# Optimization experiments

Measured on AMD Instinct MI355X. Metric: run time of the kernel, lower is better.

The kernel has to match this reference:

```python
import jax, jax.numpy as jnp
import numpy as np
import math

B, H, S, D = 4, 16, 2048, 128

def setup_inputs() -> dict:
    key = jax.random.key(0)
    kq, kk, kv = jax.random.split(key, 3)
    Q = jax.random.normal(kq, (B, H, S, D), dtype=jnp.float32)
    K = jax.random.normal(kk, (B, H, S, D), dtype=jnp.float32)
    V = jax.random.normal(kv, (B, H, S, D), dtype=jnp.float32)
    return {"Q": Q, "K": K, "V": V}

def reference(Q, K, V):
    # scores: [B, H, S, S]
    scale = 1.0 / math.sqrt(Q.shape[-1])
    scores = jnp.einsum('bhqd,bhkd->bhqk', Q, K) * scale
    attn = jax.nn.softmax(scores, axis=-1)
    return jnp.einsum('bhqk,bhkd->bhqd', attn, V)
```

## Files before the change

kernel.cpp:

```cpp
#include <hip/hip_runtime.h>
#include <stdint.h>

#define BATCH 4
#define HEADS 16
#define SEQ 2048
#define DIM 128

constexpr int QBLK  = 256;
constexpr int KVB   = 64;
constexpr int NKT   = SEQ / KVB;
constexpr int TILEB = KVB * DIM * 2;
constexpr int NBH   = BATCH * HEADS;

constexpr int K0 = 0;
constexpr int K1 = 16384;
constexpr int K2 = 32768;
constexpr int V0 = 49152;
constexpr int V1 = 65536;
constexpr int V2 = 81920;

typedef __bf16 bf16x8 __attribute__((ext_vector_type(8)));
typedef float  f32x4  __attribute__((ext_vector_type(4)));
typedef float  f32x16 __attribute__((ext_vector_type(16)));
typedef unsigned int uint32;

typedef const __attribute__((address_space(1))) void* gas_t;
typedef __attribute__((address_space(3))) void* las_t;

__device__ __forceinline__ uint32 packbf2(float a, float b) {
  union { __bf16 h[2]; uint32 u; } c;
  c.h[0] = (__bf16)a; c.h[1] = (__bf16)b;
  return c.u;
}

__global__ __launch_bounds__(256)
void prepass(const float* __restrict__ Kg, const float* __restrict__ Vg,
             char* __restrict__ Kws, char* __restrict__ Vws)
{
  __shared__ __bf16 sVt[DIM * 72];
  const int tile = blockIdx.x;
  const int tid  = threadIdx.x;
  const float* Ksrc = Kg + (size_t)tile * KVB * DIM;
  const float* Vsrc = Vg + (size_t)tile * KVB * DIM;
  char* kdst = Kws + (size_t)tile * TILEB;
  char* vdst = Vws + (size_t)tile * TILEB;

#pragma unroll
  for (int c = 0; c < 4; ++c) {
    const int flat8 = (c * 256 + tid) * 8;
    const int kv = flat8 >> 7, d0 = flat8 & 127;
    union { float4 f; float a[4]; } x0, x1;
    x0.f = *(const float4*)(Ksrc + flat8);
    x1.f = *(const float4*)(Ksrc + flat8 + 4);
    bf16x8 kx;
#pragma unroll
    for (int j = 0; j < 4; ++j) { kx[j] = (__bf16)x0.a[j]; kx[4 + j] = (__bf16)x1.a[j]; }
    *(bf16x8*)(kdst + kv * 256 + ((2 * d0) ^ ((kv & 15) << 4))) = kx;

    union { float4 f; float a[4]; } v0, v1;
    v0.f = *(const float4*)(Vsrc + flat8);
    v1.f = *(const float4*)(Vsrc + flat8 + 4);
#pragma unroll
    for (int j = 0; j < 8; ++j) {
      const int d = d0 + j;
      const float vv = (j < 4) ? v0.a[j] : v1.a[j - 4];
      sVt[d * 72 + (kv ^ (((d >> 3) & 7) << 3))] = (__bf16)vv;
    }
  }
  __syncthreads();
#pragma unroll
  for (int c = 0; c < 4; ++c) {
    const int flat8 = (c * 256 + tid) * 8;
    const int d = flat8 >> 6, kv0 = flat8 & 63;
    bf16x8 row = *(const bf16x8*)(&sVt[d * 72 + (kv0 ^ (((d >> 3) & 7) << 3))]);
    *(bf16x8*)(vdst + (d & 63) * 256 +
               ((((d >> 6) << 7) | (2 * kv0)) ^ (((d & 63) & 15) << 4))) = row;
  }
}


#define QK_HALF(KOFF)                                                            \
  {                                                                              \
    s = (f32x16)0.0f;                                                            \
    __builtin_amdgcn_s_setprio(1);                                               \
    _Pragma("unroll")                                                            \
    for (int k = 0; k < 8; ++k) {                                                \
      bf16x8 kf = *(const bf16x8*)(smem + (KOFF) + akv[k]);                      \
      s = __builtin_amdgcn_mfma_f32_32x32x16_bf16(kf, qf[k], s, 0, 0, 0);        \
    }                                                                            \
    __builtin_amdgcn_s_setprio(0);                                               \
  }

#define PV_BODY(VOFF)                                                            \
  {                                                                              \
    __builtin_amdgcn_s_setprio(1);                                               \
    _Pragma("unroll")                                                            \
    for (int td = 0; td < 4; ++td) {                                             \
      _Pragma("unroll")                                                          \
      for (int k = 0; k < 4; ++k) {                                              \
        const int ab = (td >> 1) ? (akv[k] ^ 128) : akv[k];                      \
        bf16x8 vf = *(const bf16x8*)(smem + (VOFF) + ab + (td & 1) * 8192);      \
        oacc[td] = __builtin_amdgcn_mfma_f32_32x32x16_bf16(vf, pb[k], oacc[td], 0, 0, 0); \
      }                                                                          \
    }                                                                            \
    __builtin_amdgcn_s_setprio(0);                                               \
  }

#define EXP_HALF(PB0)                                                            \
  {                                                                              \
    uint32 pk[8];                                                                \
    float rs = 0.f;                                                              \
    _Pragma("unroll")                                                            \
    for (int i = 0; i < 8; ++i) {                                                \
      float a0 = __builtin_amdgcn_exp2f(s[2*i]);                                 \
      float a1 = __builtin_amdgcn_exp2f(s[2*i+1]);                               \
      rs += a0 + a1;                                                             \
      pk[i] = packbf2(a0, a1);                                                   \
    }                                                                            \
    lrp += rs;                                                                   \
    _Pragma("unroll")                                                            \
    for (int h = 0; h < 2; ++h) {                                                \
      auto r0 = __builtin_amdgcn_permlane32_swap((int)pk[h*4+0], (int)pk[h*4+2], false, false); \
      auto r1 = __builtin_amdgcn_permlane32_swap((int)pk[h*4+1], (int)pk[h*4+3], false, false); \
      union { uint32 u[4]; bf16x8 v; } w;                                        \
      w.u[0] = (uint32)r0[0]; w.u[1] = (uint32)r1[0];                            \
      w.u[2] = (uint32)r0[1]; w.u[3] = (uint32)r1[1];                            \
      pb[(PB0) + h] = w.v;                                                       \
    }                                                                            \
  }

#define STAGE_K(DST, kt)                                                         \
  do {                                                                           \
    const char* p_ = Kt + (size_t)(kt) * TILEB;                                  \
    _Pragma("unroll")                                                            \
    for (int c_ = 0; c_ < 2; ++c_) {                                             \
      const int od_ = c_ * 8192 + wid * 1024;                                    \
      __builtin_amdgcn_global_load_lds((gas_t)(p_ + od_ + lane * 16),            \
                                       (las_t)(smem + (DST) + od_), 16, 0, 0);   \
    }                                                                            \
  } while (0)

#define STAGE_V(DST, kt)                                                         \
  do {                                                                           \
    const char* p_ = Vt + (size_t)(kt) * TILEB;                                  \
    _Pragma("unroll")                                                            \
    for (int c_ = 0; c_ < 2; ++c_) {                                             \
      const int od_ = c_ * 8192 + wid * 1024;                                    \
      __builtin_amdgcn_global_load_lds((gas_t)(p_ + od_ + lane * 16),            \
                                       (las_t)(smem + (DST) + od_), 16, 0, 0);   \
    }                                                                            \
  } while (0)

#define CBAR(VMN)                                                                \
  asm volatile("s_waitcnt vmcnt(" #VMN ")" ::: "memory");                        \
  __builtin_amdgcn_s_barrier();                                                  \
  __builtin_amdgcn_sched_barrier(0);

#define PHASE(T, KR, VR, KW, VW, DOK, DOV, VMN)                                  \
  {                                                                              \
    if (DOK) STAGE_K(KW, (T) + 2);                                               \
    if (DOV) STAGE_V(VW, (T) + 1);                                               \
    QK_HALF(KR)                                                                  \
    PV_BODY(VR)                                                                  \
    EXP_HALF(0)                                                                  \
    QK_HALF((KR) + 8192)                                                         \
    EXP_HALF(2)                                                                  \
    CBAR(VMN)                                                                    \
  }

__global__ __launch_bounds__(512, 2)
void attn_fwd(const float* __restrict__ Qg, float* __restrict__ Og,
              const char* __restrict__ Kws, const char* __restrict__ Vws)
{
  __shared__ __align__(16) char smem[98304];

  const int tid  = threadIdx.x;
  const int lane = tid & 63;
  const int wid  = tid >> 6;
  const int l    = lane & 31;
  const int hi   = lane >> 5;

  const int bid = blockIdx.x;
  const int swz = ((bid & 7) << 6) + (bid >> 3);
  const int bh  = swz >> 3;
  const int qb  = swz & 7;

  const float* Qb = Qg + (size_t)bh * SEQ * DIM;
  float*       Ob = Og + (size_t)bh * SEQ * DIM;
  const char*  Kt = Kws + (size_t)bh * NKT * TILEB;
  const char*  Vt = Vws + (size_t)bh * NKT * TILEB;

  const int q0 = qb * QBLK + wid * 32;

  int akv[8];
#pragma unroll
  for (int k = 0; k < 8; ++k)
    akv[k] = l * 256 + ((k * 32 + hi * 16) ^ ((l & 15) << 4));

  const float qscale = 0.08838834764831845f * 1.4426950408889634f;
  bf16x8 qf[8];
  {
    const float* qrow = Qb + (size_t)(q0 + l) * DIM;
#pragma unroll
    for (int k = 0; k < 8; ++k) {
      const int d0 = k * 16 + hi * 8;
      union { float4 f; float a[4]; } x0, x1;
      x0.f = *(const float4*)(qrow + d0);
      x1.f = *(const float4*)(qrow + d0 + 4);
      bf16x8 f;
#pragma unroll
      for (int j = 0; j < 4; ++j) {
        f[j]     = (__bf16)(x0.a[j] * qscale);
        f[4 + j] = (__bf16)(x1.a[j] * qscale);
      }
      qf[k] = f;
    }
  }

  float lrp = 0.f;
  f32x16 s;
  bf16x8 pb[4];
  f32x16 oacc[4];
#pragma unroll
  for (int t = 0; t < 4; ++t) oacc[t] = (f32x16)0.0f;

  STAGE_K(K0, 0);
  STAGE_K(K1, 1);
  STAGE_V(V0, 0);
  CBAR(4)

  {
    STAGE_K(K2, 2);
    STAGE_V(V1, 1);
    QK_HALF(K0)
    EXP_HALF(0)
    QK_HALF(K0 + 8192)
    EXP_HALF(2)
    CBAR(4)
  }

#pragma unroll 1
  for (int b = 1; b <= 25; b += 3) {
    PHASE(b + 0, K1, V0, K0, V2, 1, 1, 4)
    PHASE(b + 1, K2, V1, K1, V0, 1, 1, 4)
    PHASE(b + 2, K0, V2, K2, V1, 1, 1, 4)
  }
  PHASE(28, K1, V0, K0, V2, 1, 1, 4)
  PHASE(29, K2, V1, K1, V0, 1, 1, 4)
  PHASE(30, K0, V2, K0, V1, 0, 1, 2)
  PHASE(31, K1, V0, K0, V0, 0, 0, 0)
  PV_BODY(V1);

  const float lrow = lrp + __shfl_xor(lrp, 32, 64);
  const float inv = 1.0f / lrow;
  float* sO = (float*)smem;
#pragma unroll
  for (int pass = 0; pass < 2; ++pass) {
    if (pass) __syncthreads();
#pragma unroll
    for (int td2 = 0; td2 < 2; ++td2) {
      const int td = pass * 2 + td2;
#pragma unroll
      for (int rq = 0; rq < 4; ++rq) {
        const int dp = td2 * 32 + rq * 8 + hi * 4;
        f32x4 o;
        o[0] = oacc[td][rq * 4 + 0] * inv;
        o[1] = oacc[td][rq * 4 + 1] * inv;
        o[2] = oacc[td][rq * 4 + 2] * inv;
        o[3] = oacc[td][rq * 4 + 3] * inv;
        *(f32x4*)(&sO[(wid * 32 + l) * 64 + (dp ^ ((l & 15) << 2))]) = o;
      }
    }
    __syncthreads();
#pragma unroll
    for (int c = 0; c < 8; ++c) {
      const int flat4 = (c * 512 + tid) * 4;
      const int q = flat4 >> 6, dp0 = flat4 & 63;
      f32x4 o = *(const f32x4*)(&sO[q * 64 + (dp0 ^ ((q & 15) << 2))]);
      *(f32x4*)(Ob + (size_t)(qb * QBLK + q) * DIM + pass * 64 + dp0) = o;
    }
  }
}

extern "C" void kernel_launch(void* const* d_in, const int* in_sizes, int n_in,
                              void* d_out, int out_size, void* d_ws, size_t ws_size,
                              hipStream_t stream) {
  const float* Q = (const float*)d_in[0];
  const float* K = (const float*)d_in[1];
  const float* V = (const float*)d_in[2];
  float* O = (float*)d_out;
  char* Kws = (char*)d_ws;
  char* Vws = Kws + (size_t)NBH * NKT * TILEB;
  prepass<<<NBH * NKT, 256, 0, stream>>>(K, V, Kws, Vws);
  attn_fwd<<<NBH * 8, 512, 0, stream>>>(Q, O, Kws, Vws);
}
```

Measured before the change: 188.5 us.

## Give each wave two 32-row query tiles and halve the block size

Each wave now handles 64 query rows as two 32-row sub-tiles that share every K and V fragment loaded from LDS. This halves LDS reads per MFMA, and the block shrinks to 4 waves (256 threads) covering the same 256-row query block. Staging loops and wait counts are adjusted for the smaller thread count. The doubled accumulators and score registers raise register pressure, and launch bounds drop to 1 block of 256 threads, which may cut occupancy and latency hiding.

```diff
diff --git a/kernel.cpp b/kernel.cpp
--- a/kernel.cpp
+++ b/kernel.cpp
@@ -79,45 +79,47 @@
 }
 
 
-#define QK_HALF(KOFF)                                                            \
+#define QK_HALF2(KOFF)                                                           \
   {                                                                              \
-    s = (f32x16)0.0f;                                                            \
+    sA = (f32x16)0.0f; sB = (f32x16)0.0f;                                        \
     __builtin_amdgcn_s_setprio(1);                                               \
     _Pragma("unroll")                                                            \
     for (int k = 0; k < 8; ++k) {                                                \
       bf16x8 kf = *(const bf16x8*)(smem + (KOFF) + akv[k]);                      \
-      s = __builtin_amdgcn_mfma_f32_32x32x16_bf16(kf, qf[k], s, 0, 0, 0);        \
+      sA = __builtin_amdgcn_mfma_f32_32x32x16_bf16(kf, qfA[k], sA, 0, 0, 0);     \
+      sB = __builtin_amdgcn_mfma_f32_32x32x16_bf16(kf, qfB[k], sB, 0, 0, 0);     \
     }                                                                            \
     __builtin_amdgcn_s_setprio(0);                                               \
   }
 
-#define PV_BODY(VOFF)                                                            \
+#define PV_BODY2(VOFF)                                                           \
   {                                                                              \
     __builtin_amdgcn_s_setprio(1);                                               \
     _Pragma("unroll")                                                            \
-    for (int td = 0; td < 4; ++td) {                                             \
+    for (int k = 0; k < 4; ++k) {                                                \
       _Pragma("unroll")                                                          \
-      for (int k = 0; k < 4; ++k) {                                              \
+      for (int td = 0; td < 4; ++td) {                                           \
         const int ab = (td >> 1) ? (akv[k] ^ 128) : akv[k];                      \
         bf16x8 vf = *(const bf16x8*)(smem + (VOFF) + ab + (td & 1) * 8192);      \
-        oacc[td] = __builtin_amdgcn_mfma_f32_32x32x16_bf16(vf, pb[k], oacc[td], 0, 0, 0); \
+        oaccA[td] = __builtin_amdgcn_mfma_f32_32x32x16_bf16(vf, pbA[k], oaccA[td], 0, 0, 0); \
+        oaccB[td] = __builtin_amdgcn_mfma_f32_32x32x16_bf16(vf, pbB[k], oaccB[td], 0, 0, 0); \
       }                                                                          \
     }                                                                            \
     __builtin_amdgcn_s_setprio(0);                                               \
   }
 
-#define EXP_HALF(PB0)                                                            \
+#define EXP_ONE(S, PB, PB0, LRP)                                                 \
   {                                                                              \
     uint32 pk[8];                                                                \
     float rs = 0.f;                                                              \
     _Pragma("unroll")                                                            \
     for (int i = 0; i < 8; ++i) {                                                \
-      float a0 = __builtin_amdgcn_exp2f(s[2*i]);                                 \
-      float a1 = __builtin_amdgcn_exp2f(s[2*i+1]);                               \
+      float a0 = __builtin_amdgcn_exp2f(S[2*i]);                                 \
+      float a1 = __builtin_amdgcn_exp2f(S[2*i+1]);                               \
       rs += a0 + a1;                                                             \
       pk[i] = packbf2(a0, a1);                                                   \
     }                                                                            \
-    lrp += rs;                                                                   \
+    LRP += rs;                                                                   \
     _Pragma("unroll")                                                            \
     for (int h = 0; h < 2; ++h) {                                                \
       auto r0 = __builtin_amdgcn_permlane32_swap((int)pk[h*4+0], (int)pk[h*4+2], false, false); \
@@ -125,7 +127,7 @@
       union { uint32 u[4]; bf16x8 v; } w;                                        \
       w.u[0] = (uint32)r0[0]; w.u[1] = (uint32)r1[0];                            \
       w.u[2] = (uint32)r0[1]; w.u[3] = (uint32)r1[1];                            \
-      pb[(PB0) + h] = w.v;                                                       \
+      PB[(PB0) + h] = w.v;                                                       \
     }                                                                            \
   }
 
@@ -133,8 +135,8 @@
   do {                                                                           \
     const char* p_ = Kt + (size_t)(kt) * TILEB;                                  \
     _Pragma("unroll")                                                            \
-    for (int c_ = 0; c_ < 2; ++c_) {                                             \
-      const int od_ = c_ * 8192 + wid * 1024;                                    \
+    for (int c_ = 0; c_ < 4; ++c_) {                                             \
+      const int od_ = c_ * 4096 + wid * 1024;                                    \
       __builtin_amdgcn_global_load_lds((gas_t)(p_ + od_ + lane * 16),            \
                                        (las_t)(smem + (DST) + od_), 16, 0, 0);   \
     }                                                                            \
@@ -144,8 +146,8 @@
   do {                                                                           \
     const char* p_ = Vt + (size_t)(kt) * TILEB;                                  \
     _Pragma("unroll")                                                            \
-    for (int c_ = 0; c_ < 2; ++c_) {                                             \
-      const int od_ = c_ * 8192 + wid * 1024;                                    \
+    for (int c_ = 0; c_ < 4; ++c_) {                                             \
+      const int od_ = c_ * 4096 + wid * 1024;                                    \
       __builtin_amdgcn_global_load_lds((gas_t)(p_ + od_ + lane * 16),            \
                                        (las_t)(smem + (DST) + od_), 16, 0, 0);   \
     }                                                                            \
@@ -160,15 +162,17 @@
   {                                                                              \
     if (DOK) STAGE_K(KW, (T) + 2);                                               \
     if (DOV) STAGE_V(VW, (T) + 1);                                               \
-    QK_HALF(KR)                                                                  \
-    PV_BODY(VR)                                                                  \
-    EXP_HALF(0)                                                                  \
-    QK_HALF((KR) + 8192)                                                         \
-    EXP_HALF(2)                                                                  \
+    QK_HALF2(KR)                                                                 \
+    PV_BODY2(VR)                                                                 \
+    EXP_ONE(sA, pbA, 0, lrpA)                                                    \
+    EXP_ONE(sB, pbB, 0, lrpB)                                                    \
+    QK_HALF2((KR) + 8192)                                                        \
+    EXP_ONE(sA, pbA, 2, lrpA)                                                    \
+    EXP_ONE(sB, pbB, 2, lrpB)                                                    \
     CBAR(VMN)                                                                    \
   }
 
-__global__ __launch_bounds__(512, 2)
+__global__ __launch_bounds__(256, 1)
 void attn_fwd(const float* __restrict__ Qg, float* __restrict__ Og,
               const char* __restrict__ Kws, const char* __restrict__ Vws)
 {
@@ -190,7 +194,7 @@
   const char*  Kt = Kws + (size_t)bh * NKT * TILEB;
   const char*  Vt = Vws + (size_t)bh * NKT * TILEB;
 
-  const int q0 = qb * QBLK + wid * 32;
+  const int q0 = qb * QBLK + wid * 64;
 
   int akv[8];
 #pragma unroll
@@ -198,61 +202,71 @@
     akv[k] = l * 256 + ((k * 32 + hi * 16) ^ ((l & 15) << 4));
 
   const float qscale = 0.08838834764831845f * 1.4426950408889634f;
-  bf16x8 qf[8];
+  bf16x8 qfA[8], qfB[8];
   {
-    const float* qrow = Qb + (size_t)(q0 + l) * DIM;
+    const float* qrowA = Qb + (size_t)(q0 + l) * DIM;
+    const float* qrowB = Qb + (size_t)(q0 + 32 + l) * DIM;
 #pragma unroll
     for (int k = 0; k < 8; ++k) {
       const int d0 = k * 16 + hi * 8;
-      union { float4 f; float a[4]; } x0, x1;
-      x0.f = *(const float4*)(qrow + d0);
-      x1.f = *(const float4*)(qrow + d0 + 4);
-      bf16x8 f;
+      union { float4 f; float a[4]; } x0, x1, y0, y1;
+      x0.f = *(const float4*)(qrowA + d0);
+      x1.f = *(const float4*)(qrowA + d0 + 4);
+      y0.f = *(const float4*)(qrowB + d0);
+      y1.f = *(const float4*)(qrowB + d0 + 4);
+      bf16x8 fa, fb;
 #pragma unroll
       for (int j = 0; j < 4; ++j) {
-        f[j]     = (__bf16)(x0.a[j] * qscale);
-        f[4 + j] = (__bf16)(x1.a[j] * qscale);
+        fa[j]     = (__bf16)(x0.a[j] * qscale);
+        fa[4 + j] = (__bf16)(x1.a[j] * qscale);
+        fb[j]     = (__bf16)(y0.a[j] * qscale);
+        fb[4 + j] = (__bf16)(y1.a[j] * qscale);
       }
-      qf[k] = f;
+      qfA[k] = fa;
+      qfB[k] = fb;
     }
   }
 
-  float lrp = 0.f;
-  f32x16 s;
-  bf16x8 pb[4];
-  f32x16 oacc[4];
-#pragma unroll
-  for (int t = 0; t < 4; ++t) oacc[t] = (f32x16)0.0f;
+  float lrpA = 0.f, lrpB = 0.f;
+  f32x16 sA, sB;
+  bf16x8 pbA[4], pbB[4];
+  f32x16 oaccA[4], oaccB[4];
+#pragma unroll
+  for (int t = 0; t < 4; ++t) { oaccA[t] = (f32x16)0.0f; oaccB[t] = (f32x16)0.0f; }
 
   STAGE_K(K0, 0);
   STAGE_K(K1, 1);
   STAGE_V(V0, 0);
-  CBAR(4)
+  CBAR(8)
 
   {
     STAGE_K(K2, 2);
     STAGE_V(V1, 1);
-    QK_HALF(K0)
-    EXP_HALF(0)
-    QK_HALF(K0 + 8192)
-    EXP_HALF(2)
-    CBAR(4)
+    QK_HALF2(K0)
+    EXP_ONE(sA, pbA, 0, lrpA)
+    EXP_ONE(sB, pbB, 0, lrpB)
+    QK_HALF2(K0 + 8192)
+    EXP_ONE(sA, pbA, 2, lrpA)
+    EXP_ONE(sB, pbB, 2, lrpB)
+    CBAR(8)
   }
 
 #pragma unroll 1
   for (int b = 1; b <= 25; b += 3) {
-    PHASE(b + 0, K1, V0, K0, V2, 1, 1, 4)
-    PHASE(b + 1, K2, V1, K1, V0, 1, 1, 4)
-    PHASE(b + 2, K0, V2, K2, V1, 1, 1, 4)
-  }
-  PHASE(28, K1, V0, K0, V2, 1, 1, 4)
-  PHASE(29, K2, V1, K1, V0, 1, 1, 4)
-  PHASE(30, K0, V2, K0, V1, 0, 1, 2)
+    PHASE(b + 0, K1, V0, K0, V2, 1, 1, 8)
+    PHASE(b + 1, K2, V1, K1, V0, 1, 1, 8)
+    PHASE(b + 2, K0, V2, K2, V1, 1, 1, 8)
+  }
+  PHASE(28, K1, V0, K0, V2, 1, 1, 8)
+  PHASE(29, K2, V1, K1, V0, 1, 1, 8)
+  PHASE(30, K0, V2, K0, V1, 0, 1, 4)
   PHASE(31, K1, V0, K0, V0, 0, 0, 0)
-  PV_BODY(V1);
-
-  const float lrow = lrp + __shfl_xor(lrp, 32, 64);
-  const float inv = 1.0f / lrow;
+  PV_BODY2(V1);
+
+  const float lrowA = lrpA + __shfl_xor(lrpA, 32, 64);
+  const float lrowB = lrpB + __shfl_xor(lrpB, 32, 64);
+  const float invA = 1.0f / lrowA;
+  const float invB = 1.0f / lrowB;
   float* sO = (float*)smem;
 #pragma unroll
   for (int pass = 0; pass < 2; ++pass) {
@@ -263,19 +277,21 @@
 #pragma unroll
       for (int rq = 0; rq < 4; ++rq) {
         const int dp = td2 * 32 + rq * 8 + hi * 4;
-        f32x4 o;
-        o[0] = oacc[td][rq * 4 + 0] * inv;
-        o[1] = oacc[td][rq * 4 + 1] * inv;
-        o[2] = oacc[td][rq * 4 + 2] * inv;
-        o[3] = oacc[td][rq * 4 + 3] * inv;
-        *(f32x4*)(&sO[(wid * 32 + l) * 64 + (dp ^ ((l & 15) << 2))]) = o;
+        f32x4 oa, ob;
+#pragma unroll
+        for (int j = 0; j < 4; ++j) {
+          oa[j] = oaccA[td][rq * 4 + j] * invA;
+          ob[j] = oaccB[td][rq * 4 + j] * invB;
+        }
+        *(f32x4*)(&sO[(wid * 64 + l) * 64 + (dp ^ ((l & 15) << 2))])      = oa;
+        *(f32x4*)(&sO[(wid * 64 + 32 + l) * 64 + (dp ^ ((l & 15) << 2))]) = ob;
       }
     }
     __syncthreads();
 #pragma unroll
-    for (int c = 0; c < 8; ++c) {
-      const int flat4 = (c * 512 + tid) * 4;
-      const int q = flat4 >> 6, dp0 = flat4 & 63;
+    for (int c = 0; c < 16; ++c) {
+      const int flat4 = (c * 256 + tid) * 4;
+      const int q = flat4 >> 4 >> 2, dp0 = flat4 & 63;
       f32x4 o = *(const f32x4*)(&sO[q * 64 + (dp0 ^ ((q & 15) << 2))]);
       *(f32x4*)(Ob + (size_t)(qb * QBLK + q) * DIM + pass * 64 + dp0) = o;
     }
@@ -292,5 +308,5 @@
   char* Kws = (char*)d_ws;
   char* Vws = Kws + (size_t)NBH * NKT * TILEB;
   prepass<<<NBH * NKT, 256, 0, stream>>>(K, V, Kws, Vws);
-  attn_fwd<<<NBH * 8, 512, 0, stream>>>(Q, O, Kws, Vws);
+  attn_fwd<<<NBH * 8, 256, 0, stream>>>(Q, O, Kws, Vws);
 }
```

Measured after the change: 195.0 us. 3.4% more time.

## Replace triple-buffered K/V pipeline with double buffering to raise occupancy

Applied to the files above, without the earlier changes.

Shrinks the LDS K/V ring from three buffers each to two, cutting shared memory from 96KB to 64KB, and raises launch bounds to target more resident blocks per CU. The prefetch distance drops from two tiles ahead to one, and the explicit vmcnt waits are replaced by __syncthreads around the compute. This trades latency hiding within a block for more blocks to hide latency across, and adds extra barriers per tile.

```diff
diff --git a/kernel.cpp b/kernel.cpp
--- a/kernel.cpp
+++ b/kernel.cpp
@@ -14,10 +14,8 @@
 
 constexpr int K0 = 0;
 constexpr int K1 = 16384;
-constexpr int K2 = 32768;
-constexpr int V0 = 49152;
-constexpr int V1 = 65536;
-constexpr int V2 = 81920;
+constexpr int V0 = 32768;
+constexpr int V1 = 49152;
 
 typedef __bf16 bf16x8 __attribute__((ext_vector_type(8)));
 typedef float  f32x4  __attribute__((ext_vector_type(4)));
@@ -151,28 +149,24 @@
     }                                                                            \
   } while (0)
 
-#define CBAR(VMN)                                                                \
-  asm volatile("s_waitcnt vmcnt(" #VMN ")" ::: "memory");                        \
-  __builtin_amdgcn_s_barrier();                                                  \
-  __builtin_amdgcn_sched_barrier(0);
-
-#define PHASE(T, KR, VR, KW, VW, DOK, DOV, VMN)                                  \
-  {                                                                              \
-    if (DOK) STAGE_K(KW, (T) + 2);                                               \
-    if (DOV) STAGE_V(VW, (T) + 1);                                               \
+#define PHASE(T, KR, VR, KW, VW, DOK)                                            \
+  {                                                                              \
+    __syncthreads();                                                             \
     QK_HALF(KR)                                                                  \
     PV_BODY(VR)                                                                  \
     EXP_HALF(0)                                                                  \
     QK_HALF((KR) + 8192)                                                         \
+    __syncthreads();                                                             \
+    if (DOK) STAGE_K(KW, (T) + 1);                                               \
+    STAGE_V(VW, (T));                                                            \
     EXP_HALF(2)                                                                  \
-    CBAR(VMN)                                                                    \
-  }
-
-__global__ __launch_bounds__(512, 2)
+  }
+
+__global__ __launch_bounds__(512, 4)
 void attn_fwd(const float* __restrict__ Qg, float* __restrict__ Og,
               const char* __restrict__ Kws, const char* __restrict__ Vws)
 {
-  __shared__ __align__(16) char smem[98304];
+  __shared__ __align__(16) char smem[65536];
 
   const int tid  = threadIdx.x;
   const int lane = tid & 63;
@@ -196,6 +190,8 @@
 #pragma unroll
   for (int k = 0; k < 8; ++k)
     akv[k] = l * 256 + ((k * 32 + hi * 16) ^ ((l & 15) << 4));
+
+  STAGE_K(K0, 0);
 
   const float qscale = 0.08838834764831845f * 1.4426950408889634f;
   bf16x8 qf[8];
@@ -224,36 +220,36 @@
 #pragma unroll
   for (int t = 0; t < 4; ++t) oacc[t] = (f32x16)0.0f;
 
-  STAGE_K(K0, 0);
+  __syncthreads();
+  QK_HALF(K0)
+  EXP_HALF(0)
+  QK_HALF(K0 + 8192)
+  __syncthreads();
   STAGE_K(K1, 1);
   STAGE_V(V0, 0);
-  CBAR(4)
-
-  {
-    STAGE_K(K2, 2);
-    STAGE_V(V1, 1);
-    QK_HALF(K0)
-    EXP_HALF(0)
-    QK_HALF(K0 + 8192)
-    EXP_HALF(2)
-    CBAR(4)
-  }
+  EXP_HALF(2)
 
 #pragma unroll 1
-  for (int b = 1; b <= 25; b += 3) {
-    PHASE(b + 0, K1, V0, K0, V2, 1, 1, 4)
-    PHASE(b + 1, K2, V1, K1, V0, 1, 1, 4)
-    PHASE(b + 2, K0, V2, K2, V1, 1, 1, 4)
-  }
-  PHASE(28, K1, V0, K0, V2, 1, 1, 4)
-  PHASE(29, K2, V1, K1, V0, 1, 1, 4)
-  PHASE(30, K0, V2, K0, V1, 0, 1, 2)
-  PHASE(31, K1, V0, K0, V0, 0, 0, 0)
-  PV_BODY(V1);
+  for (int b = 1; b <= 29; b += 2) {
+    PHASE(b + 0, K1, V0, K0, V1, 1)
+    PHASE(b + 1, K0, V1, K1, V0, 1)
+  }
+
+  __syncthreads();
+  QK_HALF(K1)
+  PV_BODY(V0)
+  EXP_HALF(0)
+  QK_HALF(K1 + 8192)
+  __syncthreads();
+  STAGE_V(V1, 31);
+  EXP_HALF(2)
+  __syncthreads();
+  PV_BODY(V1)
 
   const float lrow = lrp + __shfl_xor(lrp, 32, 64);
   const float inv = 1.0f / lrow;
   float* sO = (float*)smem;
+  __syncthreads();
 #pragma unroll
   for (int pass = 0; pass < 2; ++pass) {
     if (pass) __syncthreads();
```

After: 493.6 us. 162% more time.
